# Optimization experiments

Hardware: AMD Instinct MI355X
Metric: run time of the kernel (lower is better)

Reference implementation:

```python
import jax, jax.numpy as jnp
import numpy as np

B, S, D = 4, 2048, 1024  # batch, steps, d_model
HEAD, DIM = 16, 64       # head*dim == D


def setup_inputs() -> dict:
    key = jax.random.key(0)
    ks = jax.random.split(key, 7)
    mk = lambda k, shp, scale: (jax.random.normal(k, shp, dtype=jnp.float32) * scale)
    w_scale = np.sqrt(2.0 / D).astype(np.float32)  # he_normal-ish
    return {
        "query": mk(ks[0], (B, S, D), 1.0),
        "key": mk(ks[1], (B, S, D), 1.0),
        "value": mk(ks[2], (B, S, D), 1.0),
        "Wq": mk(ks[3], (D, HEAD * DIM), w_scale),
        "Wk": mk(ks[4], (D, HEAD * DIM), w_scale),
        "Wv": mk(ks[5], (D, HEAD * DIM), w_scale),
        "Wo": mk(ks[6], (HEAD * DIM, D), w_scale),
    }


def reference(query, key, value, Wq, Wk, Wv, Wo):
    # Projections (heads are NOT split in the original module)
    Q = jnp.einsum('bsd,de->bse', query, Wq)   # [B,S,head*dim]
    K = jnp.einsum('bsd,de->bse', key, Wk)
    V = jnp.einsum('bsd,de->bse', value, Wv)
    scale = jnp.asarray(1.0 / np.sqrt(DIM), dtype=Q.dtype)
    scores = jnp.einsum('bqe,bke->bqk', Q, K) * scale  # [B,Sq,Sk]
    # Faithful quirk: softmax over axis=1 (the query axis), as in the source
    attn = jax.nn.softmax(scores, axis=1)
    head = jnp.einsum('bqk,bke->bqe', attn, V)  # [B,S,head*dim]
    return jnp.einsum('bqe,ed->bqd', head, Wo)  # [B,S,D]
```

## Files before the change

kernel.cpp:

```cpp
#include <hip/hip_runtime.h>


typedef _Float16 f16;
typedef _Float16 f16x8 __attribute__((ext_vector_type(8)));
typedef float f32x4 __attribute__((ext_vector_type(4)));

__device__ __forceinline__ void gl_lds16(const void* g, void* l) {
  __builtin_amdgcn_global_load_lds(
      (const __attribute__((address_space(1))) void*)(uintptr_t)g,
      (__attribute__((address_space(3))) void*)(uint32_t)(uintptr_t)l, 16, 0, 0);
}

__device__ __forceinline__ int xcd_swz(int F, int nwg) {
  int q = nwg >> 3, r = nwg & 7;
  int xcd = F & 7, idx = F >> 3;
  return (xcd < r ? xcd * (q + 1) : r * (q + 1) + (xcd - r) * q) + idx;
}

template <int EPI, int STATS, int SWZ>
__global__ __launch_bounds__(256) void gemm16(
    const f16* __restrict__ Ag, const f16* __restrict__ Bg,
    float* __restrict__ Cf, f16* __restrict__ Ch,
    float* __restrict__ pm, float* __restrict__ pl,
    int K, int ldA, int ldB, int ldC, long sA, long sB, long sC, float scale) {
  __shared__ f16 sA_[128 * 64];
  __shared__ f16 sB_[128 * 64];

  const int tid = threadIdx.x;
  const int lane = tid & 63;
  const int wave = tid >> 6;
  int bx, by;
  long bz;
  if constexpr (SWZ) {
    const int gx = gridDim.x, gy = gridDim.y;
    const int nwg = gx * gy * gridDim.z;
    int F = blockIdx.x + gx * (blockIdx.y + gy * blockIdx.z);
    int wg = xcd_swz(F, nwg);
    bx = wg % gx;
    by = (wg / gx) % gy;
    bz = wg / (gx * gy);
  } else {
    bx = blockIdx.x;
    by = blockIdx.y;
    bz = blockIdx.z;
  }

  const int tM = by * 128;
  const int tN = bx * 128;
  const int wr = (wave >> 1) * 64;
  const int wc = (wave & 1) * 64;
  const int r16 = lane & 15;
  const int q4 = lane >> 4;

  const f16* Abase = Ag + bz * sA;
  const f16* Bbase = Bg + bz * sB;

  f32x4 acc[4][4] = {};

  for (int kt = 0; kt < K; kt += 64) {
#pragma unroll
    for (int it = 0; it < 4; ++it) {
      int row = it * 32 + (tid >> 3);
      int s = tid & 7;
      int gcol = kt + ((s ^ (row & 7)) << 3);
      int lo = row * 64 + s * 8;
      gl_lds16(Abase + (long)(tM + row) * ldA + gcol, sA_ + lo);
      gl_lds16(Bbase + (long)(tN + row) * ldB + gcol, sB_ + lo);
    }
    __syncthreads();
#pragma unroll
    for (int kk = 0; kk < 2; ++kk) {
      f16x8 ah[4], bh[4];
#pragma unroll
      for (int m = 0; m < 4; ++m) {
        int ar = wr + m * 16 + r16;
        ah[m] = *(const f16x8*)(sA_ + ar * 64 + (((kk * 4 + q4) ^ (ar & 7)) << 3));
      }
#pragma unroll
      for (int n = 0; n < 4; ++n) {
        int br = wc + n * 16 + r16;
        bh[n] = *(const f16x8*)(sB_ + br * 64 + (((kk * 4 + q4) ^ (br & 7)) << 3));
      }
#pragma unroll
      for (int m = 0; m < 4; ++m)
#pragma unroll
        for (int n = 0; n < 4; ++n)
          acc[m][n] = __builtin_amdgcn_mfma_f32_16x16x32_f16(ah[m], bh[n], acc[m][n], 0, 0, 0);
    }
    __syncthreads();
  }

#pragma unroll
  for (int m = 0; m < 4; ++m)
#pragma unroll
    for (int n = 0; n < 4; ++n)
#pragma unroll
      for (int j = 0; j < 4; ++j) {
        int rr = tM + wr + m * 16 + q4 * 4 + j;
        int cc = tN + wc + n * 16 + r16;
        float v = acc[m][n][j] * scale;
        if constexpr (EPI == 0) {
          Cf[bz * sC + (long)rr * ldC + cc] = v;
        } else if constexpr (EPI == 2) {
          Ch[bz * sC + (long)rr * ldC + cc] = (f16)v;
        } else {
          if (bz == 1)
            Ch[sC + (long)cc * 2048 + (long)(rr >> 11) * 2097152L + (rr & 2047)] = (f16)v;
          else
            Ch[(long)rr * ldC + cc] = (f16)v;
        }
      }

  if constexpr (STATS) {
    float* mbuf = (float*)sA_;
    float* lbuf = mbuf + 256;
    const int wrIdx = wave >> 1, c0 = wc;
#pragma unroll
    for (int n = 0; n < 4; ++n) {
      float mt = -1e30f;
#pragma unroll
      for (int m = 0; m < 4; ++m)
#pragma unroll
        for (int j = 0; j < 4; ++j) mt = fmaxf(mt, acc[m][n][j] * scale);
      float lt = 0.f;
#pragma unroll
      for (int m = 0; m < 4; ++m)
#pragma unroll
        for (int j = 0; j < 4; ++j) lt += __expf(acc[m][n][j] * scale - mt);
#pragma unroll
      for (int d = 16; d <= 32; d <<= 1) {
        float mo = __shfl_xor(mt, d);
        float lo = __shfl_xor(lt, d);
        float mn = fmaxf(mt, mo);
        lt = lt * __expf(mt - mn) + lo * __expf(mo - mn);
        mt = mn;
      }
      if (q4 == 0) {
        int c = c0 + n * 16 + r16;
        mbuf[wrIdx * 128 + c] = mt;
        lbuf[wrIdx * 128 + c] = lt;
      }
    }
    __syncthreads();
    if (tid < 128) {
      float m0 = mbuf[tid], m1 = mbuf[128 + tid];
      float l0 = lbuf[tid], l1 = lbuf[128 + tid];
      float mn = fmaxf(m0, m1);
      float ln = l0 * __expf(m0 - mn) + l1 * __expf(m1 - mn);
      long idx = (bz * 16 + (tM >> 7)) * 2048 + tN + tid;
      pm[idx] = mn;
      pl[idx] = ln;
    }
  }
}

__global__ __launch_bounds__(256) void gemm_fold(
    const f16* __restrict__ Ag, const f16* __restrict__ Bg, f16* __restrict__ Ch,
    int K, int ldA, int ldB, int ldC, long sA, long sB, long sC) {
  __shared__ f16 sA_[128 * 64];
  __shared__ f16 sB_[128 * 64];
  const int tid = threadIdx.x;
  const int lane = tid & 63;
  const int wave = tid >> 6;
  const long bz = blockIdx.z;
  const int tM = blockIdx.y * 128;
  const int tN = blockIdx.x * 128;
  const int wr = (wave >> 1) * 64;
  const int wc = (wave & 1) * 64;
  const int r16 = lane & 15;
  const int q4 = lane >> 4;
  const f16* Abase = Ag + bz * sA;
  const f16* Bbase = Bg + bz * sB;
  f32x4 acc[4][4] = {};
  for (int kt = 0; kt < K; kt += 64) {
#pragma unroll
    for (int it = 0; it < 4; ++it) {
      int row = it * 32 + (tid >> 3);
      int s = tid & 7;
      int gcol = kt + ((s ^ (row & 7)) << 3);
      int lo = row * 64 + s * 8;
      gl_lds16(Abase + (long)(tM + row) * ldA + gcol, sA_ + lo);
      gl_lds16(Bbase + (long)(tN + row) * ldB + gcol, sB_ + lo);
    }
    __syncthreads();
#pragma unroll
    for (int kk = 0; kk < 2; ++kk) {
      f16x8 ah[4], bh[4];
#pragma unroll
      for (int m = 0; m < 4; ++m) {
        int ar = wr + m * 16 + r16;
        ah[m] = *(const f16x8*)(sA_ + ar * 64 + (((kk * 4 + q4) ^ (ar & 7)) << 3));
      }
#pragma unroll
      for (int n = 0; n < 4; ++n) {
        int br = wc + n * 16 + r16;
        bh[n] = *(const f16x8*)(sB_ + br * 64 + (((kk * 4 + q4) ^ (br & 7)) << 3));
      }
#pragma unroll
      for (int m = 0; m < 4; ++m)
#pragma unroll
        for (int n = 0; n < 4; ++n)
          acc[m][n] = __builtin_amdgcn_mfma_f32_16x16x32_f16(ah[m], bh[n], acc[m][n], 0, 0, 0);
    }
    __syncthreads();
  }
#pragma unroll
  for (int m = 0; m < 4; ++m)
#pragma unroll
    for (int n = 0; n < 4; ++n)
#pragma unroll
      for (int j = 0; j < 4; ++j) {
        int rr = tM + wr + m * 16 + q4 * 4 + j;
        int cc = tN + wc + n * 16 + r16;
        Ch[bz * sC + (long)cc * ldC + rr] = (f16)acc[m][n][j];
      }
}

__global__ __launch_bounds__(256) void convert6(
    const float* __restrict__ i0, const float* __restrict__ i1,
    const float* __restrict__ i2, const float* __restrict__ i3,
    const float* __restrict__ i4, const float* __restrict__ i5,
    f16* __restrict__ o0, f16* __restrict__ o1, f16* __restrict__ o2,
    f16* __restrict__ o3, f16* __restrict__ o4, f16* __restrict__ o5,
    long nbig, long nsmall) {
  const int z = blockIdx.z;
  const float* in;
  f16* hi;
  long n;
  switch (z) {
    case 0: in = i0; hi = o0; n = nbig; break;
    case 1: in = i1; hi = o1; n = nbig; break;
    case 2: in = i2; hi = o2; n = nbig; break;
    case 3: in = i3; hi = o3; n = nsmall; break;
    case 4: in = i4; hi = o4; n = nsmall; break;
    default: in = i5; hi = o5; n = nsmall; break;
  }
  long i = ((long)blockIdx.x * 256 + threadIdx.x) * 8;
  if (i >= n) return;
  float4 aa = *(const float4*)(in + i);
  float4 bb = *(const float4*)(in + i + 4);
  f16x8 h;
  h[0] = (f16)aa.x; h[1] = (f16)aa.y; h[2] = (f16)aa.z; h[3] = (f16)aa.w;
  h[4] = (f16)bb.x; h[5] = (f16)bb.y; h[6] = (f16)bb.z; h[7] = (f16)bb.w;
  *(f16x8*)(hi + i) = h;
}

__global__ void tconv(const float* __restrict__ in, f16* __restrict__ hi, int n) {
  __shared__ float t[32][33];
  int bx = blockIdx.x * 32, by = blockIdx.y * 32;
  int tx = threadIdx.x, ty = threadIdx.y;
  for (int i = 0; i < 32; i += 8) t[ty + i][tx] = in[(long)(by + ty + i) * n + bx + tx];
  __syncthreads();
  for (int i = 0; i < 32; i += 8)
    hi[(long)(bx + ty + i) * n + by + tx] = (f16)t[tx][ty + i];
}

__global__ void stats2(const float* __restrict__ pm, const float* __restrict__ pl,
                       float* __restrict__ mfo, float* __restrict__ rlo) {
  int c = blockIdx.x * 256 + threadIdx.x;
  int b = c >> 11, k = c & 2047;
  float m = -1e30f;
  for (int qc = 0; qc < 16; ++qc) m = fmaxf(m, pm[(b * 16 + qc) * 2048 + k]);
  float l = 0.f;
  for (int qc = 0; qc < 16; ++qc)
    l += pl[(b * 16 + qc) * 2048 + k] * __expf(pm[(b * 16 + qc) * 2048 + k] - m);
  mfo[c] = m;
  rlo[c] = 1.f / l;
}

__global__ __launch_bounds__(256) void norm(f16* __restrict__ S16,
                                            const float* __restrict__ mf,
                                            const float* __restrict__ rl) {
  long row = blockIdx.x;
  int b = (int)(row >> 11);
  f16* Sr = S16 + row * 2048;
  const float* mb = mf + ((long)b << 11);
  const float* rb = rl + ((long)b << 11);
  int c = threadIdx.x * 8;
  f16x8 v = *(f16x8*)(Sr + c);
  float4 m0 = *(const float4*)(mb + c);
  float4 m1 = *(const float4*)(mb + c + 4);
  float4 r0 = *(const float4*)(rb + c);
  float4 r1 = *(const float4*)(rb + c + 4);
  f16x8 o;
  o[0] = (f16)(__expf((float)v[0] - m0.x) * r0.x);
  o[1] = (f16)(__expf((float)v[1] - m0.y) * r0.y);
  o[2] = (f16)(__expf((float)v[2] - m0.z) * r0.z);
  o[3] = (f16)(__expf((float)v[3] - m0.w) * r0.w);
  o[4] = (f16)(__expf((float)v[4] - m1.x) * r1.x);
  o[5] = (f16)(__expf((float)v[5] - m1.y) * r1.y);
  o[6] = (f16)(__expf((float)v[6] - m1.z) * r1.z);
  o[7] = (f16)(__expf((float)v[7] - m1.w) * r1.w);
  *(f16x8*)(Sr + c) = o;
}

extern "C" void kernel_launch(void* const* d_in, const int* in_sizes, int n_in,
                              void* d_out, int out_size, void* d_ws, size_t ws_size,
                              hipStream_t stream) {
  const float* query = (const float*)d_in[0];
  const float* key   = (const float*)d_in[1];
  const float* value = (const float*)d_in[2];
  const float* Wq    = (const float*)d_in[3];
  const float* Wk    = (const float*)d_in[4];
  const float* Wv    = (const float*)d_in[5];
  const float* Wo    = (const float*)d_in[6];
  float* out = (float*)d_out;

  f16* h = (f16*)d_ws;
  const long E8 = 8388608L;
  const long E1 = 1048576L;
  f16* q16   = h;
  f16* v16   = h + E8;
  f16* k16   = h + 2 * E8;
  f16* Th    = h + 3 * E8;
  f16* VWoT  = h + 4 * E8;
  f16* WB    = h + 5 * E8;
  f16* Wq16  = WB;
  f16* wv16  = WB + E1;
  f16* Wk16  = WB + 2 * E1;
  f16* Wot   = WB + 3 * E1;
  f16* W2T   = WB + 4 * E1;
  f16* Wvot  = WB + 5 * E1;
  f16* S16   = WB + 6 * E1;
  float* pm  = (float*)(S16 + 16777216L);
  float* pl  = pm + 131072;
  float* mf  = pl + 131072;
  float* rl  = mf + 8192;
  (void)in_sizes; (void)n_in; (void)out_size; (void)ws_size;

  dim3 tb32(32, 8);
  tconv<<<dim3(32, 32), tb32, 0, stream>>>(Wo, Wot, 1024);

  convert6<<<dim3(4096, 1, 6), 256, 0, stream>>>(
      query, key, value, Wq, Wk, Wv, q16, k16, v16, Wq16, Wk16, wv16, E8, E1);

  gemm_fold<<<dim3(8, 8, 2), 256, 0, stream>>>(
      Wq16, Wk16, W2T, 1024, 1024, 1024, 1024, E1, E1, E1);

  gemm16<4, 0, 0><<<dim3(8, 64, 2), 256, 0, stream>>>(
      q16, W2T, nullptr, Th, nullptr, nullptr,
      1024, 1024, 1024, 1024, E8, E1, E8, 1.f);

  gemm16<2, 1, 1><<<dim3(16, 16, 4), 256, 0, stream>>>(
      Th, k16, nullptr, S16, pm, pl,
      1024, 1024, 1024, 2048, 2097152L, 2097152L, 4194304L, 0.125f);

  stats2<<<32, 256, 0, stream>>>(pm, pl, mf, rl);
  norm<<<8192, 256, 0, stream>>>(S16, mf, rl);

  gemm16<0, 0, 1><<<dim3(8, 16, 4), 256, 0, stream>>>(
      S16, VWoT, out, nullptr, nullptr, nullptr,
      2048, 2048, 2048, 1024, 4194304L, 2097152L, 2097152L, 1.f);
}
```

Before: 239.4 us.

## Fuse score GEMM with column softmax via cooperative grid sync

```diff
diff --git a/kernel.cpp b/kernel.cpp
--- a/kernel.cpp
+++ b/kernel.cpp
@@ -1,4 +1,7 @@
 #include <hip/hip_runtime.h>
+#include <hip/hip_cooperative_groups.h>
+
+namespace cg = cooperative_groups;
 
 
 typedef _Float16 f16;
@@ -99,16 +102,10 @@
         int rr = tM + wr + m * 16 + q4 * 4 + j;
         int cc = tN + wc + n * 16 + r16;
         float v = acc[m][n][j] * scale;
-        if constexpr (EPI == 0) {
+        if constexpr (EPI == 0)
           Cf[bz * sC + (long)rr * ldC + cc] = v;
-        } else if constexpr (EPI == 2) {
+        else
           Ch[bz * sC + (long)rr * ldC + cc] = (f16)v;
-        } else {
-          if (bz == 1)
-            Ch[sC + (long)cc * 2048 + (long)(rr >> 11) * 2097152L + (rr & 2047)] = (f16)v;
-          else
-            Ch[(long)rr * ldC + cc] = (f16)v;
-        }
       }
 
   if constexpr (STATS) {
@@ -154,33 +151,47 @@
   }
 }
 
-__global__ __launch_bounds__(256) void gemm_fold(
-    const f16* __restrict__ Ag, const f16* __restrict__ Bg, f16* __restrict__ Ch,
-    int K, int ldA, int ldB, int ldC, long sA, long sB, long sC) {
+__global__ __launch_bounds__(256) void gemm_proj(
+    const f16* __restrict__ q16, const f16* __restrict__ W2T, f16* __restrict__ Th,
+    const f16* __restrict__ Wvot, const f16* __restrict__ v16, f16* __restrict__ VWoT) {
   __shared__ f16 sA_[128 * 64];
   __shared__ f16 sB_[128 * 64];
   const int tid = threadIdx.x;
   const int lane = tid & 63;
   const int wave = tid >> 6;
-  const long bz = blockIdx.z;
-  const int tM = blockIdx.y * 128;
-  const int tN = blockIdx.x * 128;
+
+  const f16* Abase;
+  const f16* Bbase;
+  f16* Cbase;
+  int tM, tN, ldC;
+  int f = blockIdx.x;
+  if (f < 512) {
+    Abase = q16; Bbase = W2T; Cbase = Th;
+    tM = (f >> 3) * 128; tN = (f & 7) * 128; ldC = 1024;
+  } else {
+    int g = f - 512, bz = g >> 7, t = g & 127;
+    Abase = Wvot;
+    Bbase = v16 + (long)bz * 2097152;
+    Cbase = VWoT + (long)bz * 2097152;
+    tM = (t >> 4) * 128; tN = (t & 15) * 128; ldC = 2048;
+  }
+
   const int wr = (wave >> 1) * 64;
   const int wc = (wave & 1) * 64;
   const int r16 = lane & 15;
   const int q4 = lane >> 4;
-  const f16* Abase = Ag + bz * sA;
-  const f16* Bbase = Bg + bz * sB;
+
   f32x4 acc[4][4] = {};
-  for (int kt = 0; kt < K; kt += 64) {
+
+  for (int kt = 0; kt < 1024; kt += 64) {
 #pragma unroll
     for (int it = 0; it < 4; ++it) {
       int row = it * 32 + (tid >> 3);
       int s = tid & 7;
       int gcol = kt + ((s ^ (row & 7)) << 3);
       int lo = row * 64 + s * 8;
-      gl_lds16(Abase + (long)(tM + row) * ldA + gcol, sA_ + lo);
-      gl_lds16(Bbase + (long)(tN + row) * ldB + gcol, sB_ + lo);
+      gl_lds16(Abase + (long)(tM + row) * 1024 + gcol, sA_ + lo);
+      gl_lds16(Bbase + (long)(tN + row) * 1024 + gcol, sB_ + lo);
     }
     __syncthreads();
 #pragma unroll
@@ -204,6 +215,7 @@
     }
     __syncthreads();
   }
+
 #pragma unroll
   for (int m = 0; m < 4; ++m)
 #pragma unroll
@@ -212,8 +224,154 @@
       for (int j = 0; j < 4; ++j) {
         int rr = tM + wr + m * 16 + q4 * 4 + j;
         int cc = tN + wc + n * 16 + r16;
-        Ch[bz * sC + (long)cc * ldC + rr] = (f16)acc[m][n][j];
-      }
+        Cbase[(long)rr * ldC + cc] = (f16)acc[m][n][j];
+      }
+}
+
+__global__ __launch_bounds__(256, 4) void gemm_scores(
+    const f16* __restrict__ Ag, const f16* __restrict__ Bg,
+    f16* __restrict__ Ch, float* __restrict__ pm, float* __restrict__ pl) {
+  __shared__ f16 sA_[128 * 64];
+  __shared__ f16 sB_[128 * 64];
+
+  const int tid = threadIdx.x;
+  const int lane = tid & 63;
+  const int wave = tid >> 6;
+  const int gx = gridDim.x, gy = gridDim.y;
+  const int nwg = gx * gy * gridDim.z;
+  int F = blockIdx.x + gx * (blockIdx.y + gy * blockIdx.z);
+  int wg = xcd_swz(F, nwg);
+  const int bx = wg % gx;
+  const int by = (wg / gx) % gy;
+  const long bz = wg / (gx * gy);
+
+  const int tM = by * 128;
+  const int tN = bx * 128;
+  const int wr = (wave >> 1) * 64;
+  const int wc = (wave & 1) * 64;
+  const int r16 = lane & 15;
+  const int q4 = lane >> 4;
+
+  const f16* Abase = Ag + bz * 2097152L;
+  const f16* Bbase = Bg + bz * 2097152L;
+  const float scale = 0.125f;
+
+  f32x4 acc[4][4] = {};
+
+  for (int kt = 0; kt < 1024; kt += 64) {
+#pragma unroll
+    for (int it = 0; it < 4; ++it) {
+      int row = it * 32 + (tid >> 3);
+      int s = tid & 7;
+      int gcol = kt + ((s ^ (row & 7)) << 3);
+      int lo = row * 64 + s * 8;
+      gl_lds16(Abase + (long)(tM + row) * 1024 + gcol, sA_ + lo);
+      gl_lds16(Bbase + (long)(tN + row) * 1024 + gcol, sB_ + lo);
+    }
+    __syncthreads();
+#pragma unroll
+    for (int kk = 0; kk < 2; ++kk) {
+      f16x8 ah[4], bh[4];
+#pragma unroll
+      for (int m = 0; m < 4; ++m) {
+        int ar = wr + m * 16 + r16;
+        ah[m] = *(const f16x8*)(sA_ + ar * 64 + (((kk * 4 + q4) ^ (ar & 7)) << 3));
+      }
+#pragma unroll
+      for (int n = 0; n < 4; ++n) {
+        int br = wc + n * 16 + r16;
+        bh[n] = *(const f16x8*)(sB_ + br * 64 + (((kk * 4 + q4) ^ (br & 7)) << 3));
+      }
+#pragma unroll
+      for (int m = 0; m < 4; ++m)
+#pragma unroll
+        for (int n = 0; n < 4; ++n)
+          acc[m][n] = __builtin_amdgcn_mfma_f32_16x16x32_f16(ah[m], bh[n], acc[m][n], 0, 0, 0);
+    }
+    __syncthreads();
+  }
+
+  {
+    float* mbuf = (float*)sA_;
+    float* lbuf = mbuf + 256;
+    const int wrIdx = wave >> 1, c0 = wc;
+#pragma unroll
+    for (int n = 0; n < 4; ++n) {
+      float mt = -1e30f;
+#pragma unroll
+      for (int m = 0; m < 4; ++m)
+#pragma unroll
+        for (int j = 0; j < 4; ++j) mt = fmaxf(mt, acc[m][n][j] * scale);
+      float lt = 0.f;
+#pragma unroll
+      for (int m = 0; m < 4; ++m)
+#pragma unroll
+        for (int j = 0; j < 4; ++j) lt += __expf(acc[m][n][j] * scale - mt);
+#pragma unroll
+      for (int d = 16; d <= 32; d <<= 1) {
+        float mo = __shfl_xor(mt, d);
+        float lo = __shfl_xor(lt, d);
+        float mn = fmaxf(mt, mo);
+        lt = lt * __expf(mt - mn) + lo * __expf(mo - mn);
+        mt = mn;
+      }
+      if (q4 == 0) {
+        int c = c0 + n * 16 + r16;
+        mbuf[wrIdx * 128 + c] = mt;
+        lbuf[wrIdx * 128 + c] = lt;
+      }
+    }
+    __syncthreads();
+    if (tid < 128) {
+      float m0 = mbuf[tid], m1 = mbuf[128 + tid];
+      float l0 = lbuf[tid], l1 = lbuf[128 + tid];
+      float mn = fmaxf(m0, m1);
+      float ln = l0 * __expf(m0 - mn) + l1 * __expf(m1 - mn);
+      long idx = (bz * 16 + by) * 2048 + tN + tid;
+      __hip_atomic_store(&pm[idx], mn, __ATOMIC_RELAXED, __HIP_MEMORY_SCOPE_AGENT);
+      __hip_atomic_store(&pl[idx], ln, __ATOMIC_RELAXED, __HIP_MEMORY_SCOPE_AGENT);
+    }
+  }
+
+  __threadfence();
+  cg::this_grid().sync();
+
+  float* mfin = (float*)sA_;
+  float* rfin = mfin + 128;
+  if (tid < 128) {
+    float vm[16], vl[16];
+    const float* pmb = pm + bz * 16 * 2048 + tN + tid;
+    const float* plb = pl + bz * 16 * 2048 + tN + tid;
+#pragma unroll
+    for (int qc = 0; qc < 16; ++qc) {
+      vm[qc] = __hip_atomic_load(&pmb[qc * 2048], __ATOMIC_RELAXED, __HIP_MEMORY_SCOPE_AGENT);
+      vl[qc] = __hip_atomic_load(&plb[qc * 2048], __ATOMIC_RELAXED, __HIP_MEMORY_SCOPE_AGENT);
+    }
+    float m = -1e30f;
+#pragma unroll
+    for (int qc = 0; qc < 16; ++qc) m = fmaxf(m, vm[qc]);
+    float l = 0.f;
+#pragma unroll
+    for (int qc = 0; qc < 16; ++qc) l += vl[qc] * __expf(vm[qc] - m);
+    mfin[tid] = m;
+    rfin[tid] = 1.f / l;
+  }
+  __syncthreads();
+
+#pragma unroll
+  for (int m = 0; m < 4; ++m)
+#pragma unroll
+    for (int n = 0; n < 4; ++n) {
+      int ccl = wc + n * 16 + r16;
+      float mm = mfin[ccl];
+      float rl = rfin[ccl];
+#pragma unroll
+      for (int j = 0; j < 4; ++j) {
+        int rr = tM + wr + m * 16 + q4 * 4 + j;
+        Ch[bz * 4194304L + (long)rr * 2048 + tN + ccl] =
+            (f16)(__expf(acc[m][n][j] * scale - mm) * rl);
+      }
+    }
 }
 
 __global__ __launch_bounds__(256) void convert6(
@@ -315,10 +473,10 @@
   f16* Th    = h + 3 * E8;
   f16* VWoT  = h + 4 * E8;
   f16* WB    = h + 5 * E8;
-  f16* Wq16  = WB;
-  f16* wv16  = WB + E1;
-  f16* Wk16  = WB + 2 * E1;
-  f16* Wot   = WB + 3 * E1;
+  f16* Wk16  = WB;
+  f16* Wot   = WB + E1;
+  f16* Wq16  = WB + 2 * E1;
+  f16* wv16  = WB + 3 * E1;
   f16* W2T   = WB + 4 * E1;
   f16* Wvot  = WB + 5 * E1;
   f16* S16   = WB + 6 * E1;
@@ -334,19 +492,31 @@
   convert6<<<dim3(4096, 1, 6), 256, 0, stream>>>(
       query, key, value, Wq, Wk, Wv, q16, k16, v16, Wq16, Wk16, wv16, E8, E1);
 
-  gemm_fold<<<dim3(8, 8, 2), 256, 0, stream>>>(
-      Wq16, Wk16, W2T, 1024, 1024, 1024, 1024, E1, E1, E1);
-
-  gemm16<4, 0, 0><<<dim3(8, 64, 2), 256, 0, stream>>>(
-      q16, W2T, nullptr, Th, nullptr, nullptr,
-      1024, 1024, 1024, 1024, E8, E1, E8, 1.f);
-
-  gemm16<2, 1, 1><<<dim3(16, 16, 4), 256, 0, stream>>>(
-      Th, k16, nullptr, S16, pm, pl,
-      1024, 1024, 1024, 2048, 2097152L, 2097152L, 4194304L, 0.125f);
-
-  stats2<<<32, 256, 0, stream>>>(pm, pl, mf, rl);
-  norm<<<8192, 256, 0, stream>>>(S16, mf, rl);
+  gemm16<2, 0, 0><<<dim3(8, 8, 2), 256, 0, stream>>>(
+      Wk16, Wq16, nullptr, W2T, nullptr, nullptr,
+      1024, 1024, 1024, 1024, E1, E1, E1, 1.f);
+
+  gemm_proj<<<dim3(1024), 256, 0, stream>>>(q16, W2T, Th, Wvot, v16, VWoT);
+
+  {
+    const f16* a = Th;
+    const f16* b = k16;
+    f16* c = S16;
+    float* pma = pm;
+    float* pla = pl;
+    void* args[] = {&a, &b, &c, &pma, &pla};
+    hipError_t ce = hipLaunchCooperativeKernel((const void*)gemm_scores,
+                                               dim3(16, 16, 4), dim3(256, 1, 1),
+                                               args, 0, stream);
+    if (ce != hipSuccess) {
+      (void)hipGetLastError();
+      gemm16<2, 1, 1><<<dim3(16, 16, 4), 256, 0, stream>>>(
+          Th, k16, nullptr, S16, pm, pl,
+          1024, 1024, 1024, 2048, 2097152L, 2097152L, 4194304L, 0.125f);
+      stats2<<<32, 256, 0, stream>>>(pm, pl, mf, rl);
+      norm<<<8192, 256, 0, stream>>>(S16, mf, rl);
+    }
+  }
 
   gemm16<0, 0, 1><<<dim3(8, 16, 4), 256, 0, stream>>>(
       S16, VWoT, out, nullptr, nullptr, nullptr,
```

After: 395.7 us. 1.65x slower.

## Merge Q-projection and V·Wo projection GEMMs into one flat-grid kernel

Applied to the files above, without the earlier changes.

```diff
diff --git a/kernel.cpp b/kernel.cpp
--- a/kernel.cpp
+++ b/kernel.cpp
@@ -99,16 +99,10 @@
         int rr = tM + wr + m * 16 + q4 * 4 + j;
         int cc = tN + wc + n * 16 + r16;
         float v = acc[m][n][j] * scale;
-        if constexpr (EPI == 0) {
+        if constexpr (EPI == 0)
           Cf[bz * sC + (long)rr * ldC + cc] = v;
-        } else if constexpr (EPI == 2) {
+        else
           Ch[bz * sC + (long)rr * ldC + cc] = (f16)v;
-        } else {
-          if (bz == 1)
-            Ch[sC + (long)cc * 2048 + (long)(rr >> 11) * 2097152L + (rr & 2047)] = (f16)v;
-          else
-            Ch[(long)rr * ldC + cc] = (f16)v;
-        }
       }
 
   if constexpr (STATS) {
@@ -154,33 +148,47 @@
   }
 }
 
-__global__ __launch_bounds__(256) void gemm_fold(
-    const f16* __restrict__ Ag, const f16* __restrict__ Bg, f16* __restrict__ Ch,
-    int K, int ldA, int ldB, int ldC, long sA, long sB, long sC) {
+__global__ __launch_bounds__(256) void gemm_proj(
+    const f16* __restrict__ q16, const f16* __restrict__ W2T, f16* __restrict__ Th,
+    const f16* __restrict__ Wvot, const f16* __restrict__ v16, f16* __restrict__ VWoT) {
   __shared__ f16 sA_[128 * 64];
   __shared__ f16 sB_[128 * 64];
   const int tid = threadIdx.x;
   const int lane = tid & 63;
   const int wave = tid >> 6;
-  const long bz = blockIdx.z;
-  const int tM = blockIdx.y * 128;
-  const int tN = blockIdx.x * 128;
+
+  const f16* Abase;
+  const f16* Bbase;
+  f16* Cbase;
+  int tM, tN, ldC;
+  int f = blockIdx.x;
+  if (f < 512) {
+    Abase = q16; Bbase = W2T; Cbase = Th;
+    tM = (f >> 3) * 128; tN = (f & 7) * 128; ldC = 1024;
+  } else {
+    int g = f - 512, bz = g >> 7, t = g & 127;
+    Abase = Wvot;
+    Bbase = v16 + (long)bz * 2097152;
+    Cbase = VWoT + (long)bz * 2097152;
+    tM = (t >> 4) * 128; tN = (t & 15) * 128; ldC = 2048;
+  }
+
   const int wr = (wave >> 1) * 64;
   const int wc = (wave & 1) * 64;
   const int r16 = lane & 15;
   const int q4 = lane >> 4;
-  const f16* Abase = Ag + bz * sA;
-  const f16* Bbase = Bg + bz * sB;
+
   f32x4 acc[4][4] = {};
-  for (int kt = 0; kt < K; kt += 64) {
+
+  for (int kt = 0; kt < 1024; kt += 64) {
 #pragma unroll
     for (int it = 0; it < 4; ++it) {
       int row = it * 32 + (tid >> 3);
       int s = tid & 7;
       int gcol = kt + ((s ^ (row & 7)) << 3);
       int lo = row * 64 + s * 8;
-      gl_lds16(Abase + (long)(tM + row) * ldA + gcol, sA_ + lo);
-      gl_lds16(Bbase + (long)(tN + row) * ldB + gcol, sB_ + lo);
+      gl_lds16(Abase + (long)(tM + row) * 1024 + gcol, sA_ + lo);
+      gl_lds16(Bbase + (long)(tN + row) * 1024 + gcol, sB_ + lo);
     }
     __syncthreads();
 #pragma unroll
@@ -204,6 +212,7 @@
     }
     __syncthreads();
   }
+
 #pragma unroll
   for (int m = 0; m < 4; ++m)
 #pragma unroll
@@ -212,7 +221,7 @@
       for (int j = 0; j < 4; ++j) {
         int rr = tM + wr + m * 16 + q4 * 4 + j;
         int cc = tN + wc + n * 16 + r16;
-        Ch[bz * sC + (long)cc * ldC + rr] = (f16)acc[m][n][j];
+        Cbase[(long)rr * ldC + cc] = (f16)acc[m][n][j];
       }
 }
 
@@ -315,10 +324,10 @@
   f16* Th    = h + 3 * E8;
   f16* VWoT  = h + 4 * E8;
   f16* WB    = h + 5 * E8;
-  f16* Wq16  = WB;
-  f16* wv16  = WB + E1;
-  f16* Wk16  = WB + 2 * E1;
-  f16* Wot   = WB + 3 * E1;
+  f16* Wk16  = WB;
+  f16* Wot   = WB + E1;
+  f16* Wq16  = WB + 2 * E1;
+  f16* wv16  = WB + 3 * E1;
   f16* W2T   = WB + 4 * E1;
   f16* Wvot  = WB + 5 * E1;
   f16* S16   = WB + 6 * E1;
@@ -334,12 +343,11 @@
   convert6<<<dim3(4096, 1, 6), 256, 0, stream>>>(
       query, key, value, Wq, Wk, Wv, q16, k16, v16, Wq16, Wk16, wv16, E8, E1);
 
-  gemm_fold<<<dim3(8, 8, 2), 256, 0, stream>>>(
-      Wq16, Wk16, W2T, 1024, 1024, 1024, 1024, E1, E1, E1);
-
-  gemm16<4, 0, 0><<<dim3(8, 64, 2), 256, 0, stream>>>(
-      q16, W2T, nullptr, Th, nullptr, nullptr,
-      1024, 1024, 1024, 1024, E8, E1, E8, 1.f);
+  gemm16<2, 0, 0><<<dim3(8, 8, 2), 256, 0, stream>>>(
+      Wk16, Wq16, nullptr, W2T, nullptr, nullptr,
+      1024, 1024, 1024, 1024, E1, E1, E1, 1.f);
+
+  gemm_proj<<<dim3(1024), 256, 0, stream>>>(q16, W2T, Th, Wvot, v16, VWoT);
 
   gemm16<2, 1, 1><<<dim3(16, 16, 4), 256, 0, stream>>>(
       Th, k16, nullptr, S16, pm, pl,
```

Result: faster. 206.6 us (-13.7%).
